# Performance work log

Hardware: AMD Instinct MI355X
Metric: run time of the kernel (lower is better)

## Reference

```python
import jax, jax.numpy as jnp
import numpy as np

N, D, F, K = 50000, 256, 256, 10


def setup_inputs() -> dict:
    key = jax.random.key(0)
    k1, k2, k3, k4, k5, k6 = jax.random.split(key, 6)
    # neighbor indices in [-1, N); -1 marks padding (masked out in forward)
    return {
        "Z1": jax.random.normal(k1, (N, D), dtype=jnp.float32),
        "Z2": jax.random.normal(k2, (N, D), dtype=jnp.float32),
        "Wr": jax.random.normal(k3, (D, F), dtype=jnp.float32),
        "Wnr": jax.random.normal(k4, (D, F), dtype=jnp.float32),
        "n1": jax.random.randint(k5, (N, K), -1, N, dtype=jnp.int64),
        "n2": jax.random.randint(k6, (N, K), -1, N, dtype=jnp.int64),
    }


def _protein(Z, nb, Wr, Wnr):
    residues_signal = Z @ Wr                      # [N, F]
    neighbors_base_signal = Z @ Wnr               # [N, F]
    mask = (nb > -1)                              # [N, K]
    # index -1 wraps to last row (as in torch), then is zeroed by the mask
    feats = neighbors_base_signal[nb] * mask[..., None].astype(Z.dtype)  # [N, K, F]
    norm = jnp.maximum(mask.sum(axis=1), 1).astype(Z.dtype)[:, None]     # [N, 1]
    neighbors_signal = feats.sum(axis=1) / norm
    return jax.nn.relu(residues_signal + neighbors_signal)


def reference(Z1, Z2, Wr, Wnr, n1, n2):
    out1 = _protein(Z1, n1, Wr, Wnr)
    out2 = _protein(Z2, n2, Wr, Wnr)
    return jnp.stack([out1, out2])  # [2, N, F]
```

## Files before the change

kernel.cpp:

```cpp
#include <hip/hip_runtime.h>
#include <hip/hip_bf16.h>
#include <hip/hip_fp8.h>

#define NNODE 50000
#define MTOT  100000
#define DIMK  512
#define NF    256
#define KNB   10

typedef unsigned short u16;
typedef float f32x4 __attribute__((ext_vector_type(4)));
typedef short bf16x8 __attribute__((ext_vector_type(8)));

__device__ __forceinline__ u16 f2bf(float f) {
    unsigned u = __builtin_bit_cast(unsigned, f);
    unsigned r = (u + 0x7fffu + ((u >> 16) & 1u)) >> 16;
    return (u16)r;
}
__device__ __forceinline__ unsigned char f2f8(float f) {
    return (unsigned char)__hip_fp8_e4m3(f).__x;
}
__device__ __forceinline__ float f8tof(unsigned char b) {
    __hip_fp8_e4m3 h;
    h.__x = (__hip_fp8_storage_t)b;
    return (float)h;
}
__device__ __forceinline__ void gload_lds16(const void* g, void* l) {
    __builtin_amdgcn_global_load_lds(
        (const __attribute__((address_space(1))) unsigned int*)g,
        (__attribute__((address_space(3))) unsigned int*)l, 16, 0, 0);
}

__global__ __launch_bounds__(256) void cast_w(const float* __restrict__ Wr,
                                              const float* __restrict__ Wnr,
                                              u16* __restrict__ WT) {
    int id = blockIdx.x * 256 + threadIdx.x;
    int n = id >> 9;
    int k = id & 511;
    float v = (k < 256) ? Wr[(size_t)k * 256 + n] : Wnr[(size_t)(k - 256) * 256 + n];
    WT[(size_t)n * 512 + k] = f2bf(v);
}

__global__ __launch_bounds__(256) void cast_z(const float* __restrict__ Z1,
                                              const float* __restrict__ Z2,
                                              u16* __restrict__ Zcat,
                                              unsigned char* __restrict__ Z8) {
    unsigned id = blockIdx.x * 256 + threadIdx.x;
    int m = id >> 5;
    int d = (id & 31) << 3;
    const float* src = (m < NNODE) ? (Z1 + (size_t)m * 256 + d)
                                   : (Z2 + (size_t)(m - NNODE) * 256 + d);
    float4 a = *(const float4*)src;
    float4 b = *(const float4*)(src + 4);
    uint4 o;
    o.x = (unsigned)f2bf(a.x) | ((unsigned)f2bf(a.y) << 16);
    o.y = (unsigned)f2bf(a.z) | ((unsigned)f2bf(a.w) << 16);
    o.z = (unsigned)f2bf(b.x) | ((unsigned)f2bf(b.y) << 16);
    o.w = (unsigned)f2bf(b.z) | ((unsigned)f2bf(b.w) << 16);
    *(uint4*)(Zcat + (size_t)m * DIMK + d) = o;
    uint2 o8;
    o8.x = (unsigned)f2f8(a.x) | ((unsigned)f2f8(a.y) << 8) |
           ((unsigned)f2f8(a.z) << 16) | ((unsigned)f2f8(a.w) << 24);
    o8.y = (unsigned)f2f8(b.x) | ((unsigned)f2f8(b.y) << 8) |
           ((unsigned)f2f8(b.z) << 16) | ((unsigned)f2f8(b.w) << 24);
    *(uint2*)(Z8 + (size_t)m * 256 + d) = o8;
}

__global__ __launch_bounds__(256) void gather_k(const int* __restrict__ n1,
                                                const int* __restrict__ n2,
                                                const unsigned char* __restrict__ Z8,
                                                u16* __restrict__ Zcat) {
    int g = blockIdx.x * 4 + (threadIdx.x >> 6);
    int lane = threadIdx.x & 63;
    int p = (g >= NNODE);
    int i = p ? (g - NNODE) : g;
    const int* nb = (p ? n2 : n1) + (size_t)i * KNB;
    int idxs[KNB];
    const int2* nb2 = (const int2*)nb;
    #pragma unroll
    for (int k = 0; k < 5; ++k) { int2 v = nb2[k]; idxs[2 * k] = v.x; idxs[2 * k + 1] = v.y; }
    const unsigned char* base = Z8 + (size_t)p * NNODE * 256 + lane * 4;
    float a0 = 0.f, a1 = 0.f, a2 = 0.f, a3 = 0.f;
    int cnt = 0;
    #pragma unroll
    for (int k = 0; k < KNB; ++k) {
        int idx = idxs[k];
        int valid = (idx > -1);
        cnt += valid;
        uchar4 v = *(const uchar4*)(base + (size_t)(valid ? idx : 0) * 256);
        float m = (float)valid;
        a0 += m * f8tof(v.x); a1 += m * f8tof(v.y);
        a2 += m * f8tof(v.z); a3 += m * f8tof(v.w);
    }
    float s = 1.0f / (float)(cnt > 0 ? cnt : 1);
    ushort4 o;
    o.x = f2bf(a0 * s); o.y = f2bf(a1 * s); o.z = f2bf(a2 * s); o.w = f2bf(a3 * s);
    *(ushort4*)(Zcat + (size_t)g * DIMK + 256 + lane * 4) = o;
}

__global__ __launch_bounds__(512, 2) void gemm_k(const u16* __restrict__ A,
                                                 const u16* __restrict__ BT,
                                                 float* __restrict__ C) {
    __shared__ u16 sA[128 * 64];
    __shared__ u16 sB[256 * 64];
    const int m0 = blockIdx.x * 128;
    const int t = threadIdx.x;
    const int lane = t & 63;
    const int w = t >> 6;
    const int wr = w >> 2, wc = w & 3;

    f32x4 acc[4][4] = {};

    for (int kt = 0; kt < DIMK; kt += 64) {
        #pragma unroll
        for (int r = 0; r < 2; ++r) {
            int c = r * 512 + t;
            int row = c >> 3;
            int kc = c & 7;
            int grow = m0 + row;
            if (grow >= MTOT) grow = MTOT - 1;
            gload_lds16(A + (size_t)grow * DIMK + kt + kc * 8, &sA[c * 8]);
        }
        #pragma unroll
        for (int r = 0; r < 4; ++r) {
            int c = r * 512 + t;
            int row = c >> 3;
            int kc = c & 7;
            gload_lds16(BT + (size_t)row * DIMK + kt + kc * 8, &sB[c * 8]);
        }
        asm volatile("s_waitcnt vmcnt(0)");
        __syncthreads();

        #pragma unroll
        for (int kk = 0; kk < 64; kk += 32) {
            bf16x8 af[4], bfr[4];
            int kq = kk + ((lane >> 4) << 3);
            #pragma unroll
            for (int i = 0; i < 4; ++i) {
                int row = wr * 64 + i * 16 + (lane & 15);
                af[i] = *(const bf16x8*)&sA[row * 64 + kq];
            }
            #pragma unroll
            for (int j = 0; j < 4; ++j) {
                int col = wc * 64 + j * 16 + (lane & 15);
                bfr[j] = *(const bf16x8*)&sB[col * 64 + kq];
            }
            #pragma unroll
            for (int i = 0; i < 4; ++i)
                #pragma unroll
                for (int j = 0; j < 4; ++j)
                    acc[i][j] = __builtin_amdgcn_mfma_f32_16x16x32_bf16(af[i], bfr[j], acc[i][j], 0, 0, 0);
        }
        __syncthreads();
    }

    #pragma unroll
    for (int i = 0; i < 4; ++i) {
        int rbase = m0 + wr * 64 + i * 16 + ((lane >> 4) << 2);
        #pragma unroll
        for (int j = 0; j < 4; ++j) {
            int col = wc * 64 + j * 16 + (lane & 15);
            #pragma unroll
            for (int q = 0; q < 4; ++q) {
                int row = rbase + q;
                if (row < MTOT) C[(size_t)row * NF + col] = fmaxf(acc[i][j][q], 0.f);
            }
        }
    }
}

extern "C" void kernel_launch(void* const* d_in, const int* in_sizes, int n_in,
                              void* d_out, int out_size, void* d_ws, size_t ws_size,
                              hipStream_t stream) {
    const float* Z1  = (const float*)d_in[0];
    const float* Z2  = (const float*)d_in[1];
    const float* Wr  = (const float*)d_in[2];
    const float* Wnr = (const float*)d_in[3];
    const int*   n1  = (const int*)d_in[4];
    const int*   n2  = (const int*)d_in[5];
    float* out = (float*)d_out;

    u16* WT   = (u16*)d_ws;
    u16* Zcat = (u16*)d_ws + 256 * 512;
    unsigned char* Z8 = (unsigned char*)d_out + ((size_t)out_size * 4 - (size_t)MTOT * 256);

    cast_w<<<512, 256, 0, stream>>>(Wr, Wnr, WT);
    cast_z<<<12500, 256, 0, stream>>>(Z1, Z2, Zcat, Z8);
    gather_k<<<25000, 256, 0, stream>>>(n1, n2, Z8, Zcat);
    gemm_k<<<782, 512, 0, stream>>>(Zcat, WT, out);
}
```

Baseline: 131.8 us.

## Fuse neighbor gather into GEMM via swizzled LDS tile for the neighbor half

```diff
diff --git a/kernel.cpp b/kernel.cpp
--- a/kernel.cpp
+++ b/kernel.cpp
@@ -4,7 +4,6 @@
 
 #define NNODE 50000
 #define MTOT  100000
-#define DIMK  512
 #define NF    256
 #define KNB   10
 
@@ -43,7 +42,7 @@
 
 __global__ __launch_bounds__(256) void cast_z(const float* __restrict__ Z1,
                                               const float* __restrict__ Z2,
-                                              u16* __restrict__ Zcat,
+                                              u16* __restrict__ Zleft,
                                               unsigned char* __restrict__ Z8) {
     unsigned id = blockIdx.x * 256 + threadIdx.x;
     int m = id >> 5;
@@ -57,7 +56,7 @@
     o.y = (unsigned)f2bf(a.z) | ((unsigned)f2bf(a.w) << 16);
     o.z = (unsigned)f2bf(b.x) | ((unsigned)f2bf(b.y) << 16);
     o.w = (unsigned)f2bf(b.z) | ((unsigned)f2bf(b.w) << 16);
-    *(uint4*)(Zcat + (size_t)m * DIMK + d) = o;
+    *(uint4*)(Zleft + (size_t)m * 256 + d) = o;
     uint2 o8;
     o8.x = (unsigned)f2f8(a.x) | ((unsigned)f2f8(a.y) << 8) |
            ((unsigned)f2f8(a.z) << 16) | ((unsigned)f2f8(a.w) << 24);
@@ -66,83 +65,80 @@
     *(uint2*)(Z8 + (size_t)m * 256 + d) = o8;
 }
 
-__global__ __launch_bounds__(256) void gather_k(const int* __restrict__ n1,
-                                                const int* __restrict__ n2,
-                                                const unsigned char* __restrict__ Z8,
-                                                u16* __restrict__ Zcat) {
-    int g = blockIdx.x * 4 + (threadIdx.x >> 6);
-    int lane = threadIdx.x & 63;
-    int p = (g >= NNODE);
-    int i = p ? (g - NNODE) : g;
-    const int* nb = (p ? n2 : n1) + (size_t)i * KNB;
-    int idxs[KNB];
-    const int2* nb2 = (const int2*)nb;
-    #pragma unroll
-    for (int k = 0; k < 5; ++k) { int2 v = nb2[k]; idxs[2 * k] = v.x; idxs[2 * k + 1] = v.y; }
-    const unsigned char* base = Z8 + (size_t)p * NNODE * 256 + lane * 4;
-    float a0 = 0.f, a1 = 0.f, a2 = 0.f, a3 = 0.f;
-    int cnt = 0;
-    #pragma unroll
-    for (int k = 0; k < KNB; ++k) {
-        int idx = idxs[k];
-        int valid = (idx > -1);
-        cnt += valid;
-        uchar4 v = *(const uchar4*)(base + (size_t)(valid ? idx : 0) * 256);
-        float m = (float)valid;
-        a0 += m * f8tof(v.x); a1 += m * f8tof(v.y);
-        a2 += m * f8tof(v.z); a3 += m * f8tof(v.w);
-    }
-    float s = 1.0f / (float)(cnt > 0 ? cnt : 1);
-    ushort4 o;
-    o.x = f2bf(a0 * s); o.y = f2bf(a1 * s); o.z = f2bf(a2 * s); o.w = f2bf(a3 * s);
-    *(ushort4*)(Zcat + (size_t)g * DIMK + 256 + lane * 4) = o;
-}
-
-__global__ __launch_bounds__(512, 2) void gemm_k(const u16* __restrict__ A,
-                                                 const u16* __restrict__ BT,
-                                                 float* __restrict__ C) {
-    __shared__ u16 sA[128 * 64];
+__global__ __launch_bounds__(256, 2) void gemm_fused(const u16* __restrict__ A,
+                                                     const unsigned char* __restrict__ Z8,
+                                                     const u16* __restrict__ BT,
+                                                     const int* __restrict__ n1,
+                                                     const int* __restrict__ n2,
+                                                     float* __restrict__ C) {
+    __shared__ u16 sA[64 * 64];
     __shared__ u16 sB[256 * 64];
-    const int m0 = blockIdx.x * 128;
+    __shared__ u16 sZ[64 * 256];
+    const int m0 = blockIdx.x * 64;
     const int t = threadIdx.x;
     const int lane = t & 63;
     const int w = t >> 6;
-    const int wr = w >> 2, wc = w & 3;
+
+    {
+        const unsigned char* zb = Z8 + lane * 4;
+        for (int rr = 0; rr < 16; ++rr) {
+            int r = w * 16 + rr;
+            int g = m0 + r;
+            if (g >= MTOT) g = MTOT - 1;
+            int p = (g >= NNODE);
+            int i = g - p * NNODE;
+            const int* nb = (p ? n2 : n1) + (size_t)i * KNB;
+            float a0 = 0.f, a1 = 0.f, a2 = 0.f, a3 = 0.f;
+            int cnt = 0;
+            #pragma unroll
+            for (int k = 0; k < KNB; ++k) {
+                int idx = nb[k];
+                int valid = (idx > -1);
+                cnt += valid;
+                uchar4 v = *(const uchar4*)(zb + (size_t)(p * NNODE + (valid ? idx : 0)) * 256);
+                float mm = (float)valid;
+                a0 += mm * f8tof(v.x); a1 += mm * f8tof(v.y);
+                a2 += mm * f8tof(v.z); a3 += mm * f8tof(v.w);
+            }
+            float s = 1.0f / (float)(cnt > 0 ? cnt : 1);
+            ushort4 o;
+            o.x = f2bf(a0 * s); o.y = f2bf(a1 * s); o.z = f2bf(a2 * s); o.w = f2bf(a3 * s);
+            int byteoff = r * 512 + ((((lane >> 1) ^ (r & 7)) << 4) | ((lane & 1) << 3));
+            *(ushort4*)((char*)sZ + byteoff) = o;
+        }
+    }
 
     f32x4 acc[4][4] = {};
 
-    for (int kt = 0; kt < DIMK; kt += 64) {
-        #pragma unroll
-        for (int r = 0; r < 2; ++r) {
-            int c = r * 512 + t;
-            int row = c >> 3;
-            int kc = c & 7;
+    for (int kt = 0; kt < 256; kt += 64) {
+        #pragma unroll
+        for (int rp = 0; rp < 2; ++rp) {
+            int c = rp * 256 + t;
+            int row = c >> 3, kc = c & 7;
             int grow = m0 + row;
             if (grow >= MTOT) grow = MTOT - 1;
-            gload_lds16(A + (size_t)grow * DIMK + kt + kc * 8, &sA[c * 8]);
-        }
-        #pragma unroll
-        for (int r = 0; r < 4; ++r) {
-            int c = r * 512 + t;
-            int row = c >> 3;
-            int kc = c & 7;
-            gload_lds16(BT + (size_t)row * DIMK + kt + kc * 8, &sB[c * 8]);
+            gload_lds16(A + (size_t)grow * 256 + kt + kc * 8, &sA[c * 8]);
+        }
+        #pragma unroll
+        for (int rp = 0; rp < 8; ++rp) {
+            int c = rp * 256 + t;
+            int col = c >> 3, kc = c & 7;
+            gload_lds16(BT + (size_t)col * 512 + kt + kc * 8, &sB[c * 8]);
         }
         asm volatile("s_waitcnt vmcnt(0)");
         __syncthreads();
-
         #pragma unroll
         for (int kk = 0; kk < 64; kk += 32) {
+            int kq = kk + ((lane >> 4) << 3);
             bf16x8 af[4], bfr[4];
-            int kq = kk + ((lane >> 4) << 3);
             #pragma unroll
             for (int i = 0; i < 4; ++i) {
-                int row = wr * 64 + i * 16 + (lane & 15);
+                int row = i * 16 + (lane & 15);
                 af[i] = *(const bf16x8*)&sA[row * 64 + kq];
             }
             #pragma unroll
             for (int j = 0; j < 4; ++j) {
-                int col = wc * 64 + j * 16 + (lane & 15);
+                int col = w * 64 + j * 16 + (lane & 15);
                 bfr[j] = *(const bf16x8*)&sB[col * 64 + kq];
             }
             #pragma unroll
@@ -154,12 +150,46 @@
         __syncthreads();
     }
 
+    for (int kt = 256; kt < 512; kt += 64) {
+        #pragma unroll
+        for (int rp = 0; rp < 8; ++rp) {
+            int c = rp * 256 + t;
+            int col = c >> 3, kc = c & 7;
+            gload_lds16(BT + (size_t)col * 512 + kt + kc * 8, &sB[c * 8]);
+        }
+        asm volatile("s_waitcnt vmcnt(0)");
+        __syncthreads();
+        #pragma unroll
+        for (int kk = 0; kk < 64; kk += 32) {
+            int kq = kk + ((lane >> 4) << 3);
+            bf16x8 af[4], bfr[4];
+            #pragma unroll
+            for (int i = 0; i < 4; ++i) {
+                int row = i * 16 + (lane & 15);
+                int kcol = (kt - 256) + kq;
+                int byteoff = row * 512 + ((((kcol >> 3) ^ (row & 7)) << 4));
+                af[i] = *(const bf16x8*)((const char*)sZ + byteoff);
+            }
+            #pragma unroll
+            for (int j = 0; j < 4; ++j) {
+                int col = w * 64 + j * 16 + (lane & 15);
+                bfr[j] = *(const bf16x8*)&sB[col * 64 + kq];
+            }
+            #pragma unroll
+            for (int i = 0; i < 4; ++i)
+                #pragma unroll
+                for (int j = 0; j < 4; ++j)
+                    acc[i][j] = __builtin_amdgcn_mfma_f32_16x16x32_bf16(af[i], bfr[j], acc[i][j], 0, 0, 0);
+        }
+        __syncthreads();
+    }
+
     #pragma unroll
     for (int i = 0; i < 4; ++i) {
-        int rbase = m0 + wr * 64 + i * 16 + ((lane >> 4) << 2);
+        int rbase = m0 + i * 16 + ((lane >> 4) << 2);
         #pragma unroll
         for (int j = 0; j < 4; ++j) {
-            int col = wc * 64 + j * 16 + (lane & 15);
+            int col = w * 64 + j * 16 + (lane & 15);
             #pragma unroll
             for (int q = 0; q < 4; ++q) {
                 int row = rbase + q;
@@ -180,12 +210,11 @@
     const int*   n2  = (const int*)d_in[5];
     float* out = (float*)d_out;
 
-    u16* WT   = (u16*)d_ws;
-    u16* Zcat = (u16*)d_ws + 256 * 512;
-    unsigned char* Z8 = (unsigned char*)d_out + ((size_t)out_size * 4 - (size_t)MTOT * 256);
+    u16* WT    = (u16*)d_ws;
+    u16* Zleft = WT + 256 * 512;
+    unsigned char* Z8 = (unsigned char*)(Zleft + (size_t)MTOT * 256);
 
     cast_w<<<512, 256, 0, stream>>>(Wr, Wnr, WT);
-    cast_z<<<12500, 256, 0, stream>>>(Z1, Z2, Zcat, Z8);
-    gather_k<<<25000, 256, 0, stream>>>(n1, n2, Z8, Zcat);
-    gemm_k<<<782, 512, 0, stream>>>(Zcat, WT, out);
-}
+    cast_z<<<12500, 256, 0, stream>>>(Z1, Z2, Zleft, Z8);
+    gemm_fused<<<1563, 256, 0, stream>>>(Zleft, Z8, WT, n1, n2, out);
+}
```

After: 148.4 us. 1.13x slower.

## Fuse neighbor gather into GEMM and use fp8 MFMA for neighbor half

Applied to the files above, without the earlier changes.

```diff
diff --git a/kernel.cpp b/kernel.cpp
--- a/kernel.cpp
+++ b/kernel.cpp
@@ -4,12 +4,12 @@
 
 #define NNODE 50000
 #define MTOT  100000
-#define DIMK  512
 #define NF    256
 #define KNB   10
 
 typedef unsigned short u16;
 typedef float f32x4 __attribute__((ext_vector_type(4)));
+typedef float f32x2 __attribute__((ext_vector_type(2)));
 typedef short bf16x8 __attribute__((ext_vector_type(8)));
 
 __device__ __forceinline__ u16 f2bf(float f) {
@@ -25,146 +25,221 @@
     h.__x = (__hip_fp8_storage_t)b;
     return (float)h;
 }
-__device__ __forceinline__ void gload_lds16(const void* g, void* l) {
-    __builtin_amdgcn_global_load_lds(
-        (const __attribute__((address_space(1))) unsigned int*)g,
-        (__attribute__((address_space(3))) unsigned int*)l, 16, 0, 0);
-}
-
-__global__ __launch_bounds__(256) void cast_w(const float* __restrict__ Wr,
-                                              const float* __restrict__ Wnr,
-                                              u16* __restrict__ WT) {
-    int id = blockIdx.x * 256 + threadIdx.x;
-    int n = id >> 9;
-    int k = id & 511;
-    float v = (k < 256) ? Wr[(size_t)k * 256 + n] : Wnr[(size_t)(k - 256) * 256 + n];
-    WT[(size_t)n * 512 + k] = f2bf(v);
-}
-
-__global__ __launch_bounds__(256) void cast_z(const float* __restrict__ Z1,
-                                              const float* __restrict__ Z2,
-                                              u16* __restrict__ Zcat,
-                                              unsigned char* __restrict__ Z8) {
-    unsigned id = blockIdx.x * 256 + threadIdx.x;
-    int m = id >> 5;
-    int d = (id & 31) << 3;
-    const float* src = (m < NNODE) ? (Z1 + (size_t)m * 256 + d)
-                                   : (Z2 + (size_t)(m - NNODE) * 256 + d);
-    float4 a = *(const float4*)src;
-    float4 b = *(const float4*)(src + 4);
-    uint4 o;
-    o.x = (unsigned)f2bf(a.x) | ((unsigned)f2bf(a.y) << 16);
-    o.y = (unsigned)f2bf(a.z) | ((unsigned)f2bf(a.w) << 16);
-    o.z = (unsigned)f2bf(b.x) | ((unsigned)f2bf(b.y) << 16);
-    o.w = (unsigned)f2bf(b.z) | ((unsigned)f2bf(b.w) << 16);
-    *(uint4*)(Zcat + (size_t)m * DIMK + d) = o;
-    uint2 o8;
-    o8.x = (unsigned)f2f8(a.x) | ((unsigned)f2f8(a.y) << 8) |
-           ((unsigned)f2f8(a.z) << 16) | ((unsigned)f2f8(a.w) << 24);
-    o8.y = (unsigned)f2f8(b.x) | ((unsigned)f2f8(b.y) << 8) |
-           ((unsigned)f2f8(b.z) << 16) | ((unsigned)f2f8(b.w) << 24);
-    *(uint2*)(Z8 + (size_t)m * 256 + d) = o8;
-}
-
-__global__ __launch_bounds__(256) void gather_k(const int* __restrict__ n1,
-                                                const int* __restrict__ n2,
-                                                const unsigned char* __restrict__ Z8,
-                                                u16* __restrict__ Zcat) {
-    int g = blockIdx.x * 4 + (threadIdx.x >> 6);
-    int lane = threadIdx.x & 63;
-    int p = (g >= NNODE);
-    int i = p ? (g - NNODE) : g;
-    const int* nb = (p ? n2 : n1) + (size_t)i * KNB;
-    int idxs[KNB];
-    const int2* nb2 = (const int2*)nb;
-    #pragma unroll
-    for (int k = 0; k < 5; ++k) { int2 v = nb2[k]; idxs[2 * k] = v.x; idxs[2 * k + 1] = v.y; }
-    const unsigned char* base = Z8 + (size_t)p * NNODE * 256 + lane * 4;
-    float a0 = 0.f, a1 = 0.f, a2 = 0.f, a3 = 0.f;
-    int cnt = 0;
+template <int WORD>
+__device__ __forceinline__ f32x2 cvt2_fp8(unsigned v) {
+#if __has_builtin(__builtin_amdgcn_cvt_pk_f32_fp8)
+    auto c = __builtin_amdgcn_cvt_pk_f32_fp8((int)v, WORD);
+    f32x2 r; r.x = c[0]; r.y = c[1];
+    return r;
+#else
+    unsigned s = WORD ? (v >> 16) : v;
+    f32x2 r;
+    r.x = f8tof((unsigned char)(s & 0xff));
+    r.y = f8tof((unsigned char)((s >> 8) & 0xff));
+    return r;
+#endif
+}
+template <int WORD>
+__device__ __forceinline__ unsigned pk_fp8(float a, float b, unsigned old) {
+#if __has_builtin(__builtin_amdgcn_cvt_pk_fp8_f32)
+    return (unsigned)__builtin_amdgcn_cvt_pk_fp8_f32(a, b, (int)old, WORD);
+#else
+    unsigned lo = (unsigned)f2f8(a) | ((unsigned)f2f8(b) << 8);
+    return WORD ? ((old & 0x0000ffffu) | (lo << 16)) : ((old & 0xffff0000u) | lo);
+#endif
+}
+
+__global__ __launch_bounds__(256) void cast_all(const float* __restrict__ Z1,
+                                                const float* __restrict__ Z2,
+                                                const float* __restrict__ Wr,
+                                                const float* __restrict__ Wnr,
+                                                u16* __restrict__ Zleft,
+                                                unsigned char* __restrict__ Z8,
+                                                u16* __restrict__ WT,
+                                                unsigned char* __restrict__ WT8) {
+    int b = blockIdx.x;
+    if (b < 12500) {
+        unsigned id = b * 256 + threadIdx.x;
+        int m = id >> 5;
+        int d = (id & 31) << 3;
+        const float* src = (m < NNODE) ? (Z1 + (size_t)m * 256 + d)
+                                       : (Z2 + (size_t)(m - NNODE) * 256 + d);
+        float4 a = *(const float4*)src;
+        float4 bb = *(const float4*)(src + 4);
+        uint4 o;
+        o.x = (unsigned)f2bf(a.x) | ((unsigned)f2bf(a.y) << 16);
+        o.y = (unsigned)f2bf(a.z) | ((unsigned)f2bf(a.w) << 16);
+        o.z = (unsigned)f2bf(bb.x) | ((unsigned)f2bf(bb.y) << 16);
+        o.w = (unsigned)f2bf(bb.z) | ((unsigned)f2bf(bb.w) << 16);
+        *(uint4*)(Zleft + (size_t)m * 256 + d) = o;
+        uint2 o8;
+        o8.x = (unsigned)f2f8(a.x) | ((unsigned)f2f8(a.y) << 8) |
+               ((unsigned)f2f8(a.z) << 16) | ((unsigned)f2f8(a.w) << 24);
+        o8.y = (unsigned)f2f8(bb.x) | ((unsigned)f2f8(bb.y) << 8) |
+               ((unsigned)f2f8(bb.z) << 16) | ((unsigned)f2f8(bb.w) << 24);
+        *(uint2*)(Z8 + (size_t)m * 256 + d) = o8;
+    } else if (b < 12756) {
+        int id = (b - 12500) * 256 + threadIdx.x;
+        int n = id >> 8, k = id & 255;
+        WT[n * 256 + k] = f2bf(Wr[(size_t)k * 256 + n]);
+    } else {
+        int id = (b - 12756) * 256 + threadIdx.x;
+        int n = id >> 8, k = id & 255;
+        WT8[n * 256 + k] = f2f8(Wnr[(size_t)k * 256 + n]);
+    }
+}
+
+__device__ __forceinline__ void consume(const uint2 (&gv)[KNB], unsigned mask, int cnt,
+                                        int w, int lane, int s, unsigned char* sZ) {
+    f32x2 a0 = {0.f, 0.f}, a1 = {0.f, 0.f}, a2 = {0.f, 0.f}, a3 = {0.f, 0.f};
     #pragma unroll
     for (int k = 0; k < KNB; ++k) {
-        int idx = idxs[k];
-        int valid = (idx > -1);
-        cnt += valid;
-        uchar4 v = *(const uchar4*)(base + (size_t)(valid ? idx : 0) * 256);
-        float m = (float)valid;
-        a0 += m * f8tof(v.x); a1 += m * f8tof(v.y);
-        a2 += m * f8tof(v.z); a3 += m * f8tof(v.w);
-    }
-    float s = 1.0f / (float)(cnt > 0 ? cnt : 1);
-    ushort4 o;
-    o.x = f2bf(a0 * s); o.y = f2bf(a1 * s); o.z = f2bf(a2 * s); o.w = f2bf(a3 * s);
-    *(ushort4*)(Zcat + (size_t)g * DIMK + 256 + lane * 4) = o;
-}
-
-__global__ __launch_bounds__(512, 2) void gemm_k(const u16* __restrict__ A,
-                                                 const u16* __restrict__ BT,
-                                                 float* __restrict__ C) {
-    __shared__ u16 sA[128 * 64];
-    __shared__ u16 sB[256 * 64];
-    const int m0 = blockIdx.x * 128;
+        float mm = (float)((mask >> k) & 1u);
+        f32x2 m2 = {mm, mm};
+        a0 += m2 * cvt2_fp8<0>(gv[k].x);
+        a1 += m2 * cvt2_fp8<1>(gv[k].x);
+        a2 += m2 * cvt2_fp8<0>(gv[k].y);
+        a3 += m2 * cvt2_fp8<1>(gv[k].y);
+    }
+    float sc = 1.0f / (float)(cnt > 0 ? cnt : 1);
+    unsigned w0 = pk_fp8<0>(a0.x * sc, a0.y * sc, 0u);
+    w0 = pk_fp8<1>(a1.x * sc, a1.y * sc, w0);
+    unsigned w1 = pk_fp8<0>(a2.x * sc, a2.y * sc, 0u);
+    w1 = pk_fp8<1>(a3.x * sc, a3.y * sc, w1);
+    int rl = w * 8 + s * 2 + (lane >> 5);
+    int gp = (lane & 31) ^ (rl & 7);
+    *(uint2*)(sZ + rl * 256 + (gp << 3)) = make_uint2(w0, w1);
+}
+
+__global__ __launch_bounds__(256, 3) void gemm_fused(const u16* __restrict__ Zl,
+                                                     const unsigned char* __restrict__ Z8,
+                                                     const u16* __restrict__ WT,
+                                                     const unsigned char* __restrict__ WT8,
+                                                     const int* __restrict__ n1,
+                                                     const int* __restrict__ n2,
+                                                     float* __restrict__ C) {
+    __shared__ unsigned char sZ[32 * 256];
+    const int m0 = (3124 - blockIdx.x) * 32;
     const int t = threadIdx.x;
     const int lane = t & 63;
     const int w = t >> 6;
-    const int wr = w >> 2, wc = w & 3;
-
-    f32x4 acc[4][4] = {};
-
-    for (int kt = 0; kt < DIMK; kt += 64) {
+    const int hi = lane >> 4;
+    const int l15 = lane & 15;
+
+    f32x4 acc[2][4] = {};
+    uint2 gv[KNB];
+    int2 icur[5], inxt[5];
+    unsigned pmask = 0;
+    int pcnt = 0;
+
+    {
+        int g = m0 + w * 8 + (lane >> 5);
+        int p = (g >= NNODE);
+        const int* nb = (p ? n2 : n1) + (size_t)(g - p * NNODE) * KNB;
         #pragma unroll
-        for (int r = 0; r < 2; ++r) {
-            int c = r * 512 + t;
-            int row = c >> 3;
-            int kc = c & 7;
-            int grow = m0 + row;
-            if (grow >= MTOT) grow = MTOT - 1;
-            gload_lds16(A + (size_t)grow * DIMK + kt + kc * 8, &sA[c * 8]);
-        }
-        #pragma unroll
-        for (int r = 0; r < 4; ++r) {
-            int c = r * 512 + t;
-            int row = c >> 3;
-            int kc = c & 7;
-            gload_lds16(BT + (size_t)row * DIMK + kt + kc * 8, &sB[c * 8]);
-        }
-        asm volatile("s_waitcnt vmcnt(0)");
-        __syncthreads();
-
-        #pragma unroll
-        for (int kk = 0; kk < 64; kk += 32) {
-            bf16x8 af[4], bfr[4];
-            int kq = kk + ((lane >> 4) << 3);
-            #pragma unroll
-            for (int i = 0; i < 4; ++i) {
-                int row = wr * 64 + i * 16 + (lane & 15);
-                af[i] = *(const bf16x8*)&sA[row * 64 + kq];
-            }
-            #pragma unroll
-            for (int j = 0; j < 4; ++j) {
-                int col = wc * 64 + j * 16 + (lane & 15);
-                bfr[j] = *(const bf16x8*)&sB[col * 64 + kq];
-            }
-            #pragma unroll
-            for (int i = 0; i < 4; ++i)
-                #pragma unroll
-                for (int j = 0; j < 4; ++j)
-                    acc[i][j] = __builtin_amdgcn_mfma_f32_16x16x32_bf16(af[i], bfr[j], acc[i][j], 0, 0, 0);
-        }
-        __syncthreads();
-    }
+        for (int q = 0; q < 5; ++q) icur[q] = *(const int2*)(nb + 2 * q);
+    }
+
+#define LSTEP(S)                                                              \
+    do {                                                                      \
+        const int kt = (S) * 64;                                              \
+        bf16x8 af[2][2], bfr[2][4];                                           \
+        _Pragma("unroll")                                                     \
+        for (int k2 = 0; k2 < 2; ++k2) {                                      \
+            int kq = kt + k2 * 32 + hi * 8;                                   \
+            _Pragma("unroll")                                                 \
+            for (int i = 0; i < 2; ++i)                                       \
+                af[k2][i] = *(const bf16x8*)(Zl + (size_t)(m0 + i * 16 + l15) * 256 + kq); \
+            _Pragma("unroll")                                                 \
+            for (int j = 0; j < 4; ++j)                                       \
+                bfr[k2][j] = *(const bf16x8*)(WT + (size_t)(w * 64 + j * 16 + l15) * 256 + kq); \
+        }                                                                     \
+        if ((S) < 3) {                                          \
+            int g = m0 + w * 8 + ((S) + 1) * 2 + (lane >> 5);                 \
+            int p = (g >= NNODE);                                             \
+            const int* nb = (p ? n2 : n1) + (size_t)(g - p * NNODE) * KNB;    \
+            _Pragma("unroll")                                                 \
+            for (int q = 0; q < 5; ++q) inxt[q] = *(const int2*)(nb + 2 * q); \
+        }                                                                     \
+        if ((S) > 0) consume(gv, pmask, pcnt, w, lane, (S) - 1, sZ);          \
+        {                                                     \
+            int g = m0 + w * 8 + (S) * 2 + (lane >> 5);                       \
+            int p = (g >= NNODE);                                             \
+            const unsigned char* zb = Z8 + (size_t)p * ((size_t)NNODE * 256) + ((lane & 31) << 3); \
+            unsigned mask = 0;                                                \
+            int cnt = 0;                                                      \
+            _Pragma("unroll")                                                 \
+            for (int k = 0; k < KNB; ++k) {                                   \
+                int ix = (k & 1) ? icur[k >> 1].y : icur[k >> 1].x;           \
+                int valid = (ix > -1) ? 1 : 0;                                \
+                mask |= (unsigned)valid << k;                                 \
+                cnt += valid;                                                 \
+                gv[k] = *(const uint2*)(zb + (size_t)(valid ? ix : 0) * 256); \
+            }                                                                 \
+            pmask = mask;                                                     \
+            pcnt = cnt;                                                       \
+        }                                                                     \
+        if ((S) < 3) {                                                        \
+            _Pragma("unroll")                                                 \
+            for (int q = 0; q < 5; ++q) icur[q] = inxt[q];                    \
+        }                                                                     \
+        _Pragma("unroll")                                                     \
+        for (int k2 = 0; k2 < 2; ++k2)                                        \
+            _Pragma("unroll")                                                 \
+            for (int i = 0; i < 2; ++i)                                       \
+                _Pragma("unroll")                                             \
+                for (int j = 0; j < 4; ++j)                                   \
+                    acc[i][j] = __builtin_amdgcn_mfma_f32_16x16x32_bf16(af[k2][i], bfr[k2][j], acc[i][j], 0, 0, 0); \
+    } while (0)
+
+    LSTEP(0);
+    LSTEP(1);
+    LSTEP(2);
+    LSTEP(3);
+#undef LSTEP
+
+    consume(gv, pmask, pcnt, w, lane, 3, sZ);
+    __syncthreads();
+
+#define RSTEP(R)                                                              \
+    do {                                                                      \
+        _Pragma("unroll")                                                     \
+        for (int m = 0; m < 2; ++m) {                                         \
+            long long az[2], bz[4];                                           \
+            _Pragma("unroll")                                                 \
+            for (int i = 0; i < 2; ++i) {                                     \
+                int row = i * 16 + l15;                                       \
+                int g8 = (R) * 8 + m * 4 + hi;                                \
+                az[i] = *(const long long*)(sZ + row * 256 + ((g8 ^ (row & 7)) << 3)); \
+            }                                                                 \
+            _Pragma("unroll")                                                 \
+            for (int j = 0; j < 4; ++j) {                                     \
+                int col = w * 64 + j * 16 + l15;                              \
+                bz[j] = *(const long long*)(WT8 + (size_t)col * 256 + (R) * 64 + m * 32 + hi * 8); \
+            }                                                                 \
+            _Pragma("unroll")                                                 \
+            for (int i = 0; i < 2; ++i)                                       \
+                _Pragma("unroll")                                             \
+                for (int j = 0; j < 4; ++j)                                   \
+                    acc[i][j] = __builtin_amdgcn_mfma_f32_16x16x32_fp8_fp8(az[i], bz[j], acc[i][j], 0, 0, 0); \
+        }                                                                     \
+    } while (0)
+
+    RSTEP(0);
+    RSTEP(1);
+    RSTEP(2);
+    RSTEP(3);
+#undef RSTEP
 
     #pragma unroll
-    for (int i = 0; i < 4; ++i) {
-        int rbase = m0 + wr * 64 + i * 16 + ((lane >> 4) << 2);
+    for (int i = 0; i < 2; ++i) {
+        int rbase = m0 + i * 16 + (hi << 2);
         #pragma unroll
         for (int j = 0; j < 4; ++j) {
-            int col = wc * 64 + j * 16 + (lane & 15);
+            int col = w * 64 + j * 16 + l15;
             #pragma unroll
-            for (int q = 0; q < 4; ++q) {
-                int row = rbase + q;
-                if (row < MTOT) C[(size_t)row * NF + col] = fmaxf(acc[i][j][q], 0.f);
-            }
+            for (int q = 0; q < 4; ++q)
+                C[(size_t)(rbase + q) * NF + col] = fmaxf(acc[i][j][q], 0.f);
         }
     }
 }
@@ -180,12 +255,11 @@
     const int*   n2  = (const int*)d_in[5];
     float* out = (float*)d_out;
 
-    u16* WT   = (u16*)d_ws;
-    u16* Zcat = (u16*)d_ws + 256 * 512;
-    unsigned char* Z8 = (unsigned char*)d_out + ((size_t)out_size * 4 - (size_t)MTOT * 256);
-
-    cast_w<<<512, 256, 0, stream>>>(Wr, Wnr, WT);
-    cast_z<<<12500, 256, 0, stream>>>(Z1, Z2, Zcat, Z8);
-    gather_k<<<25000, 256, 0, stream>>>(n1, n2, Z8, Zcat);
-    gemm_k<<<782, 512, 0, stream>>>(Zcat, WT, out);
-}
+    u16* WT            = (u16*)d_ws;
+    unsigned char* WT8 = (unsigned char*)d_ws + 131072;
+    u16* Zleft         = (u16*)((unsigned char*)d_ws + 196608);
+    unsigned char* Z8  = (unsigned char*)d_ws + 196608 + (size_t)MTOT * 512;
+
+    cast_all<<<13012, 256, 0, stream>>>(Z1, Z2, Wr, Wnr, Zleft, Z8, WT, WT8);
+    gemm_fused<<<3125, 256, 0, stream>>>(Zleft, Z8, WT, WT8, n1, n2, out);
+}
```

Result: slower. 175.7 us (+33.3%).
